# Kernel optimization log

Measured on AMD Instinct MI355X. Metric: run time of the kernel, lower is better.

The kernel has to match this reference:

```python
import jax, jax.numpy as jnp
import numpy as np

N_NODES = 100000

def _sage_conv(x, src, dst, deg_inv, Wl, bl, Wr):
    # PyG SAGEConv (aggr='mean', root_weight=True):
    #   out = lin_l(mean_{j in N(i)} x_j) + lin_r(x_i)
    msg = x[src]                                            # [E, d]
    agg = jax.ops.segment_sum(msg, dst, num_segments=N_NODES)  # [N, d]
    agg = agg * deg_inv                                     # mean (0 for isolated nodes)
    return agg @ Wl.T + bl + x @ Wr.T


def setup_inputs() -> dict:
    key = jax.random.key(0)
    ks = jax.random.split(key, 12)
    N, E, d_in, d_h, d_out = N_NODES, 1600000, 64, 64, 32
    x = jax.random.normal(ks[0], (N, d_in), dtype=jnp.float32)
    edge_index = jax.random.randint(ks[1], (2, E), 0, N, dtype=jnp.int64)

    def glorot(k, shape):
        fan_in = shape[1]
        return jax.random.normal(k, shape, dtype=jnp.float32) / np.sqrt(fan_in)

    return {
        "x": x,
        "edge_index": edge_index,
        "W1l": glorot(ks[2], (d_h, d_in)), "b1l": jnp.zeros((d_h,), jnp.float32), "W1r": glorot(ks[3], (d_h, d_in)),
        "W2l": glorot(ks[4], (d_h, d_h)),  "b2l": jnp.zeros((d_h,), jnp.float32), "W2r": glorot(ks[5], (d_h, d_h)),
        "W3l": glorot(ks[6], (d_h, d_h)),  "b3l": jnp.zeros((d_h,), jnp.float32), "W3r": glorot(ks[7], (d_h, d_h)),
        "Wfc": glorot(ks[8], (d_out, d_h)), "bfc": jnp.zeros((d_out,), jnp.float32),
    }


def reference(x, edge_index, W1l, b1l, W1r, W2l, b2l, W2r, W3l, b3l, W3r, Wfc, bfc):
    src, dst = edge_index[0], edge_index[1]
    # in-degree per destination node (shared by all three conv layers)
    ones = jnp.ones((src.shape[0],), x.dtype)
    deg = jax.ops.segment_sum(ones, dst, num_segments=N_NODES)
    deg_inv = (1.0 / jnp.maximum(deg, 1.0))[:, None]        # [N, 1]

    h = jax.nn.relu(_sage_conv(x, src, dst, deg_inv, W1l, b1l, W1r))
    # dropout(p=0.5) is identity in eval mode
    h = jax.nn.relu(_sage_conv(h, src, dst, deg_inv, W2l, b2l, W2r))
    h = jax.nn.relu(_sage_conv(h, src, dst, deg_inv, W3l, b3l, W3r))
    return h @ Wfc.T + bfc
```

## Files before the change

kernel.cpp:

```cpp
#include <hip/hip_runtime.h>
#include <hip/hip_fp16.h>

#define N_NODES 100000
#define D 64
#define BR 256
#define NB 391
#define ECH 2560
#define NROWPAD 100096

typedef _Float16 f16x8 __attribute__((ext_vector_type(8)));
typedef float f32x4 __attribute__((ext_vector_type(4)));

__device__ __forceinline__ float rlf(float v, int l) {
    union { float f; int i; } u;
    u.f = v;
    u.i = __builtin_amdgcn_readlane(u.i, l);
    return u.f;
}

__global__ __launch_bounds__(256) void k_cvt(const float4* __restrict__ x,
                                             uint2* __restrict__ y, int n4) {
    int i = blockIdx.x * 256 + threadIdx.x;
    if (i < n4) {
        float4 v = x[i];
        union { __half2 h[2]; uint2 u; } pk;
        pk.h[0] = __floats2half2_rn(v.x, v.y);
        pk.h[1] = __floats2half2_rn(v.z, v.w);
        y[i] = pk.u;
    }
}

__global__ __launch_bounds__(256) void k_prep(const float* __restrict__ Wl1, const float* __restrict__ Wr1,
                                              const float* __restrict__ Wl2, const float* __restrict__ Wr2,
                                              const float* __restrict__ Wl3, const float* __restrict__ Wr3,
                                              const float* __restrict__ Wfc,
                                              __half* __restrict__ Wf1, __half* __restrict__ Wf2,
                                              __half* __restrict__ Wf3, __half* __restrict__ Wffc,
                                              unsigned* __restrict__ x16, unsigned* __restrict__ H1,
                                              unsigned* __restrict__ H2,
                                              int* __restrict__ histT, int padded) {
    int t = blockIdx.x * 256 + threadIdx.x;
    if (t < 24576) {
        int layer = t / 8192;
        int r = t % 8192;
        int f = r >> 9, rem = r & 511;
        int lane = rem >> 3, i = rem & 7;
        int kt = f >> 2, nt = f & 3;
        int k = kt * 32 + (lane >> 4) * 8 + i;
        int o = nt * 16 + (lane & 15);
        const float* Wl = layer == 0 ? Wl1 : layer == 1 ? Wl2 : Wl3;
        const float* Wr = layer == 0 ? Wr1 : layer == 1 ? Wr2 : Wr3;
        float v = (k < 64) ? Wl[o * 64 + k] : Wr[o * 64 + (k - 64)];
        __half* Wf = layer == 0 ? Wf1 : layer == 1 ? Wf2 : Wf3;
        Wf[r] = __float2half(v);
    } else if (t < 26624) {
        int r = t - 24576;
        int f = r >> 9, rem = r & 511;
        int lane = rem >> 3, i = rem & 7;
        int kt = f >> 1, nt = f & 1;
        int k = kt * 32 + (lane >> 4) * 8 + i;
        int o = nt * 16 + (lane & 15);
        Wffc[r] = __float2half(Wfc[o * 64 + k]);
    } else if (t < 26720) {
        int z = t - 26624;
        unsigned* buf = (z >> 5) == 0 ? x16 : (z >> 5) == 1 ? H1 : H2;
        buf[(size_t)N_NODES * 32 + (z & 31)] = 0u;
    } else if (t >= 32768 && t < 32768 + padded) {
        histT[t - 32768] = 0;
    }
}


__global__ __launch_bounds__(512) void k_hist(const int* __restrict__ dst,
                                              int* __restrict__ histT,
                                              int E, int ga) {
    __shared__ int h[NB];
    int blk = blockIdx.x, tid = threadIdx.x;
    for (int i = tid; i < NB; i += 512) h[i] = 0;
    __syncthreads();
    int base = blk * ECH;
    int lim = E - base; if (lim > ECH) lim = ECH;
    for (int i = tid; i < lim; i += 512)
        atomicAdd(&h[dst[base + i] >> 8], 1);
    __syncthreads();
    for (int i = tid; i < NB; i += 512)
        histT[i * ga + blk] = h[i];
}

__global__ __launch_bounds__(256) void k_scan1(const int* __restrict__ cnt,
                                               int* __restrict__ part,
                                               int* __restrict__ bsums) {
    __shared__ int s[256];
    int tid = threadIdx.x;
    int i4 = blockIdx.x * 256 + tid;
    int4 v = reinterpret_cast<const int4*>(cnt)[i4];
    int tsum = v.x + v.y + v.z + v.w;
    s[tid] = tsum;
    __syncthreads();
    for (int off = 1; off < 256; off <<= 1) {
        int t = 0;
        if (tid >= off) t = s[tid - off];
        __syncthreads();
        if (tid >= off) s[tid] += t;
        __syncthreads();
    }
    int excl = tid ? s[tid - 1] : 0;
    if (tid == 255) bsums[blockIdx.x] = s[255];
    int4 o;
    o.x = excl;
    o.y = o.x + v.x;
    o.z = o.y + v.y;
    o.w = o.z + v.z;
    reinterpret_cast<int4*>(part)[i4] = o;
}

__global__ __launch_bounds__(256) void k_scan2(int* __restrict__ bsums, int nb,
                                               int* __restrict__ col) {
    __shared__ int s[256];
    int tid = threadIdx.x;
    if (tid < 8) col[tid] = N_NODES;
    int v = (tid < nb) ? bsums[tid] : 0;
    s[tid] = v;
    __syncthreads();
    for (int off = 1; off < 256; off <<= 1) {
        int t = 0;
        if (tid >= off) t = s[tid - off];
        __syncthreads();
        if (tid >= off) s[tid] += t;
        __syncthreads();
    }
    if (tid < nb) bsums[tid] = tid ? s[tid - 1] : 0;
}

__global__ __launch_bounds__(512) void k_part(const int* __restrict__ src,
                                              const int* __restrict__ dst,
                                              const int* __restrict__ offs,
                                              const int* __restrict__ bsums,
                                              int* __restrict__ bedge,
                                              int E, int ga) {
    __shared__ int o[NB];
    int blk = blockIdx.x, tid = threadIdx.x;
    for (int i = tid; i < NB; i += 512) {
        int ent = i * ga + blk;
        o[i] = offs[ent] + bsums[ent >> 10];
    }
    __syncthreads();
    int base = blk * ECH;
    int lim = E - base; if (lim > ECH) lim = ECH;
    for (int i = tid; i < lim; i += 512) {
        int e = base + i;
        int d = dst[e];
        int pos = atomicAdd(&o[d >> 8], 1);
        bedge[pos] = src[e] | ((d & 255) << 17);
    }
}

__global__ __launch_bounds__(256) void k_csr(const int* __restrict__ bedge,
                                             const int* __restrict__ offs,
                                             const int* __restrict__ bsums,
                                             int* __restrict__ col,
                                             int2* __restrict__ rp,
                                             float* __restrict__ deg_inv,
                                             int E, int ga) {
    __shared__ int lcnt[BR];
    __shared__ int stmp[BR];
    __shared__ int lcur[BR];
    int b = blockIdx.x, tid = threadIdx.x;
    int e0 = b * ga;
    int ebeg = offs[e0] + bsums[e0 >> 10];
    int eend = E;
    if (b + 1 < NB) {
        int e1 = (b + 1) * ga;
        eend = offs[e1] + bsums[e1 >> 10];
    }
    int nbase = b * BR;
    int cbase = ebeg + b * (BR * 4) + 8;
    lcnt[tid] = 0;
    __syncthreads();
    for (int e = ebeg + tid; e < eend; e += 256)
        atomicAdd(&lcnt[bedge[e] >> 17], 1);
    __syncthreads();
    int v = lcnt[tid];
    int pdeg = (v + 3) & ~3;
    stmp[tid] = pdeg;
    __syncthreads();
    for (int off = 1; off < 256; off <<= 1) {
        int t = 0;
        if (tid >= off) t = stmp[tid - off];
        __syncthreads();
        if (tid >= off) stmp[tid] += t;
        __syncthreads();
    }
    int ex = tid ? stmp[tid - 1] : 0;
    int slot = cbase + ex;
    lcur[tid] = slot;
    int node = nbase + tid;
    if (node < N_NODES) {
        rp[node] = make_int2(slot, slot + pdeg);
        deg_inv[node] = 1.0f / (float)(v > 1 ? v : 1);
        for (int s2 = slot + v; s2 < slot + pdeg; ++s2) col[s2] = N_NODES;
    }
    __syncthreads();
    for (int e = ebeg + tid; e < eend; e += 256) {
        int ed = bedge[e];
        int pos = atomicAdd(&lcur[ed >> 17], 1);
        col[pos] = ed & 0x1FFFF;
    }
}


__device__ __forceinline__ void fused_core(const __half* __restrict__ Hin,
                                           const __half* __restrict__ Wf,
                                           const float* __restrict__ bias,
                                           const int2* __restrict__ rp,
                                           const int* __restrict__ col,
                                           const float* __restrict__ deg_inv, int n,
                                           __half (&lds)[16][72], int m0, int l,
                                           f32x4 (&acc)[4]) {
    int q = l >> 4, li = l & 15;
    int beg = 0, nq = 0;
    float dinv = 0.f;
    if (l < 16 && m0 + l < n) {
        int2 se = rp[m0 + l];
        beg = se.x;
        nq = (se.y - se.x) >> 2;
        dinv = deg_inv[m0 + l];
    }
    const uint2* x8 = (const uint2*)Hin;
    const int* cq = col + q;

#pragma unroll
    for (int g = 0; g < 4; ++g) {
        int b0 = __builtin_amdgcn_readlane(beg, 4 * g + 0);
        int b1 = __builtin_amdgcn_readlane(beg, 4 * g + 1);
        int b2 = __builtin_amdgcn_readlane(beg, 4 * g + 2);
        int b3 = __builtin_amdgcn_readlane(beg, 4 * g + 3);
        int c0 = __builtin_amdgcn_readlane(nq, 4 * g + 0);
        int c1 = __builtin_amdgcn_readlane(nq, 4 * g + 1);
        int c2 = __builtin_amdgcn_readlane(nq, 4 * g + 2);
        int c3 = __builtin_amdgcn_readlane(nq, 4 * g + 3);
        int qmax = max(max(c0, c1), max(c2, c3));
        __half2 s00 = __floats2half2_rn(0.f, 0.f), s01 = s00;
        __half2 s10 = s00, s11 = s00, s20 = s00, s21 = s00, s30 = s00, s31 = s00;
        for (int qq = 0; qq < qmax; qq += 2) {
            int o = qq * 4;
            int a0 = qq < c0 ? b0 + o : 0;
            int a1 = qq < c1 ? b1 + o : 0;
            int a2 = qq < c2 ? b2 + o : 0;
            int a3 = qq < c3 ? b3 + o : 0;
            int a4 = qq + 1 < c0 ? b0 + o + 4 : 0;
            int a5 = qq + 1 < c1 ? b1 + o + 4 : 0;
            int a6 = qq + 1 < c2 ? b2 + o + 4 : 0;
            int a7 = qq + 1 < c3 ? b3 + o + 4 : 0;
            int i0 = cq[a0], i1 = cq[a1], i2 = cq[a2], i3 = cq[a3];
            int i4 = cq[a4], i5 = cq[a5], i6 = cq[a6], i7 = cq[a7];
            uint2 u0 = x8[(size_t)i0 * 16 + li];
            uint2 u1 = x8[(size_t)i1 * 16 + li];
            uint2 u2 = x8[(size_t)i2 * 16 + li];
            uint2 u3 = x8[(size_t)i3 * 16 + li];
            uint2 u4 = x8[(size_t)i4 * 16 + li];
            uint2 u5 = x8[(size_t)i5 * 16 + li];
            uint2 u6 = x8[(size_t)i6 * 16 + li];
            uint2 u7 = x8[(size_t)i7 * 16 + li];
            union { unsigned v; __half2 h; } w;
            w.v = u0.x; s00 = __hadd2(s00, w.h);
            w.v = u0.y; s01 = __hadd2(s01, w.h);
            w.v = u1.x; s10 = __hadd2(s10, w.h);
            w.v = u1.y; s11 = __hadd2(s11, w.h);
            w.v = u2.x; s20 = __hadd2(s20, w.h);
            w.v = u2.y; s21 = __hadd2(s21, w.h);
            w.v = u3.x; s30 = __hadd2(s30, w.h);
            w.v = u3.y; s31 = __hadd2(s31, w.h);
            w.v = u4.x; s00 = __hadd2(s00, w.h);
            w.v = u4.y; s01 = __hadd2(s01, w.h);
            w.v = u5.x; s10 = __hadd2(s10, w.h);
            w.v = u5.y; s11 = __hadd2(s11, w.h);
            w.v = u6.x; s20 = __hadd2(s20, w.h);
            w.v = u6.y; s21 = __hadd2(s21, w.h);
            w.v = u7.x; s30 = __hadd2(s30, w.h);
            w.v = u7.y; s31 = __hadd2(s31, w.h);
        }
        union { __half2 h; int i; } t;
#pragma unroll
        for (int m = 16; m < 64; m <<= 1) {
            t.h = s00; t.i = __shfl_xor(t.i, m); s00 = __hadd2(s00, t.h);
            t.h = s01; t.i = __shfl_xor(t.i, m); s01 = __hadd2(s01, t.h);
            t.h = s10; t.i = __shfl_xor(t.i, m); s10 = __hadd2(s10, t.h);
            t.h = s11; t.i = __shfl_xor(t.i, m); s11 = __hadd2(s11, t.h);
            t.h = s20; t.i = __shfl_xor(t.i, m); s20 = __hadd2(s20, t.h);
            t.h = s21; t.i = __shfl_xor(t.i, m); s21 = __hadd2(s21, t.h);
            t.h = s30; t.i = __shfl_xor(t.i, m); s30 = __hadd2(s30, t.h);
            t.h = s31; t.i = __shfl_xor(t.i, m); s31 = __hadd2(s31, t.h);
        }
        float d0 = rlf(dinv, 4 * g + 0);
        float d1 = rlf(dinv, 4 * g + 1);
        float d2 = rlf(dinv, 4 * g + 2);
        float d3 = rlf(dinv, 4 * g + 3);
        if (l < 16) {
            union { __half2 h; unsigned v; } p0, p1;
            float2 f;
            uint2 ov;
            f = __half22float2(s00); p0.h = __floats2half2_rn(f.x * d0, f.y * d0);
            f = __half22float2(s01); p1.h = __floats2half2_rn(f.x * d0, f.y * d0);
            ov.x = p0.v; ov.y = p1.v;
            *(uint2*)&lds[4 * g + 0][li * 4] = ov;
            f = __half22float2(s10); p0.h = __floats2half2_rn(f.x * d1, f.y * d1);
            f = __half22float2(s11); p1.h = __floats2half2_rn(f.x * d1, f.y * d1);
            ov.x = p0.v; ov.y = p1.v;
            *(uint2*)&lds[4 * g + 1][li * 4] = ov;
            f = __half22float2(s20); p0.h = __floats2half2_rn(f.x * d2, f.y * d2);
            f = __half22float2(s21); p1.h = __floats2half2_rn(f.x * d2, f.y * d2);
            ov.x = p0.v; ov.y = p1.v;
            *(uint2*)&lds[4 * g + 2][li * 4] = ov;
            f = __half22float2(s30); p0.h = __floats2half2_rn(f.x * d3, f.y * d3);
            f = __half22float2(s31); p1.h = __floats2half2_rn(f.x * d3, f.y * d3);
            ov.x = p0.v; ov.y = p1.v;
            *(uint2*)&lds[4 * g + 3][li * 4] = ov;
        }
    }

    const f16x8* wf8 = (const f16x8*)Wf;
    f16x8 bf[4][4];
#pragma unroll
    for (int kt = 0; kt < 4; ++kt)
#pragma unroll
        for (int nt = 0; nt < 4; ++nt)
            bf[kt][nt] = wf8[(kt * 4 + nt) * 64 + l];
    int rowA = li;
#pragma unroll
    for (int nt = 0; nt < 4; ++nt) {
        float bs = bias[nt * 16 + rowA];
        acc[nt] = (f32x4){bs, bs, bs, bs};
    }
#pragma unroll
    for (int kt = 0; kt < 4; ++kt) {
        f16x8 a;
        if (kt < 2)
            a = *(const f16x8*)&lds[rowA][kt * 32 + q * 8];
        else
            a = *(const f16x8*)(Hin + (size_t)(m0 + rowA) * D + (kt - 2) * 32 + q * 8);
#pragma unroll
        for (int nt = 0; nt < 4; ++nt)
            acc[nt] = __builtin_amdgcn_mfma_f32_16x16x32_f16(a, bf[kt][nt], acc[nt], 0, 0, 0);
    }
}

__global__ __launch_bounds__(256) void k_fused(const __half* __restrict__ Hin,
                                               __half* __restrict__ Hout,
                                               const __half* __restrict__ Wf,
                                               const float* __restrict__ bias,
                                               const int2* __restrict__ rp,
                                               const int* __restrict__ col,
                                               const float* __restrict__ deg_inv, int n) {
    __shared__ __half lds[4][16][72];
    int l = threadIdx.x & 63;
    int wv = threadIdx.x >> 6;
    int m0 = blockIdx.x * 64 + wv * 16;
    f32x4 acc[4];
    fused_core(Hin, Wf, bias, rp, col, deg_inv, n, lds[wv], m0, l, acc);
    int q = l >> 4, rowA = l & 15;
#pragma unroll
    for (int nt = 0; nt < 4; ++nt)
#pragma unroll
        for (int qd = 0; qd < 4; ++qd) {
            int node = m0 + q * 4 + qd;
            float v = fmaxf(acc[nt][qd], 0.f);
            if (node < n)
                Hout[(size_t)node * D + nt * 16 + rowA] = __float2half(v);
        }
}

__global__ __launch_bounds__(256) void k_fused_fc(const __half* __restrict__ Hin,
                                                  float* __restrict__ out,
                                                  const __half* __restrict__ Wf,
                                                  const float* __restrict__ bias,
                                                  const __half* __restrict__ Wffc,
                                                  const float* __restrict__ bfc,
                                                  const int2* __restrict__ rp,
                                                  const int* __restrict__ col,
                                                  const float* __restrict__ deg_inv, int n) {
    __shared__ __half lds[4][16][72];
    int l = threadIdx.x & 63;
    int wv = threadIdx.x >> 6;
    int m0 = blockIdx.x * 64 + wv * 16;
    f32x4 acc[4];
    fused_core(Hin, Wf, bias, rp, col, deg_inv, n, lds[wv], m0, l, acc);
    int q = l >> 4, li = l & 15;

#pragma unroll
    for (int nt = 0; nt < 4; ++nt)
#pragma unroll
        for (int qd = 0; qd < 4; ++qd)
            lds[wv][q * 4 + qd][nt * 16 + li] = __float2half(fmaxf(acc[nt][qd], 0.f));

    const f16x8* wfc8 = (const f16x8*)Wffc;
    f16x8 bf2[2][2];
#pragma unroll
    for (int kt = 0; kt < 2; ++kt)
#pragma unroll
        for (int nt = 0; nt < 2; ++nt)
            bf2[kt][nt] = wfc8[(kt * 2 + nt) * 64 + l];
    f32x4 acc2[2];
#pragma unroll
    for (int nt = 0; nt < 2; ++nt) {
        float bs = bfc[nt * 16 + li];
        acc2[nt] = (f32x4){bs, bs, bs, bs};
    }
#pragma unroll
    for (int kt = 0; kt < 2; ++kt) {
        f16x8 a = *(const f16x8*)&lds[wv][li][kt * 32 + q * 8];
#pragma unroll
        for (int nt = 0; nt < 2; ++nt)
            acc2[nt] = __builtin_amdgcn_mfma_f32_16x16x32_f16(a, bf2[kt][nt], acc2[nt], 0, 0, 0);
    }
#pragma unroll
    for (int nt = 0; nt < 2; ++nt)
#pragma unroll
        for (int qd = 0; qd < 4; ++qd) {
            int node = m0 + q * 4 + qd;
            if (node < n)
                out[(size_t)node * 32 + nt * 16 + li] = acc2[nt][qd];
        }
}


extern "C" void kernel_launch(void* const* d_in, const int* in_sizes, int n_in,
                              void* d_out, int out_size, void* d_ws, size_t ws_size,
                              hipStream_t stream) {
    const float* x   = (const float*)d_in[0];
    const int*   ei  = (const int*)d_in[1];
    const int    E   = in_sizes[1] / 2;
    const int*   src = ei;
    const int*   dst = ei + E;
    const float* W1l = (const float*)d_in[2];
    const float* b1l = (const float*)d_in[3];
    const float* W1r = (const float*)d_in[4];
    const float* W2l = (const float*)d_in[5];
    const float* b2l = (const float*)d_in[6];
    const float* W2r = (const float*)d_in[7];
    const float* W3l = (const float*)d_in[8];
    const float* b3l = (const float*)d_in[9];
    const float* W3r = (const float*)d_in[10];
    const float* Wfc = (const float*)d_in[11];
    const float* bfc = (const float*)d_in[12];
    float* out = (float*)d_out;

    const int ga      = (E + ECH - 1) / ECH;
    const int entries = NB * ga;
    const int padded  = (entries + 1023) & ~1023;
    const int nb2     = padded / 1024;

    char* p = (char*)d_ws;
    size_t off = 0;
    auto take = [&](size_t bytes) -> void* {
        void* r = p + off;
        off = (off + bytes + 255) & ~(size_t)255;
        return r;
    };
    __half* x16    = (__half*)take((size_t)NROWPAD * D * 2);
    __half* H1     = (__half*)take((size_t)NROWPAD * D * 2);
    __half* H2     = (__half*)take((size_t)NROWPAD * D * 2);
    float* deg_inv = (float*)take((size_t)N_NODES * 4);
    int2*  rp      = (int2*)take((size_t)N_NODES * 8);
    int*   histT   = (int*)take((size_t)padded * 4);
    int*   offs    = (int*)take((size_t)padded * 4);
    int*   bsums   = (int*)take(256 * 4);
    int*   bedge   = (int*)take((size_t)E * 4);
    int*   col     = (int*)take((size_t)(E + NB * BR * 4 + 72) * 4);
    __half* Wf1    = (__half*)take(8192 * 2);
    __half* Wf2    = (__half*)take(8192 * 2);
    __half* Wf3    = (__half*)take(8192 * 2);
    __half* Wffc   = (__half*)take(2048 * 2);

    int gp = (32768 + padded + 255) / 256;
    k_prep<<<gp, 256, 0, stream>>>(W1l, W1r, W2l, W2r, W3l, W3r, Wfc,
                                   Wf1, Wf2, Wf3, Wffc,
                                   (unsigned*)x16, (unsigned*)H1, (unsigned*)H2,
                                   histT, padded);
    int n4 = N_NODES * D / 4;
    k_cvt<<<(n4 + 255) / 256, 256, 0, stream>>>((const float4*)x, (uint2*)x16, n4);

    k_hist<<<ga, 512, 0, stream>>>(dst, histT, E, ga);
    k_scan1<<<nb2, 256, 0, stream>>>(histT, offs, bsums);
    k_scan2<<<1, 256, 0, stream>>>(bsums, nb2, col);
    k_part<<<ga, 512, 0, stream>>>(src, dst, offs, bsums, bedge, E, ga);
    k_csr<<<NB, 256, 0, stream>>>(bedge, offs, bsums, col, rp, deg_inv, E, ga);

    int gg = NROWPAD / 64;

    k_fused<<<gg, 256, 0, stream>>>(x16, H1, Wf1, b1l, rp, col, deg_inv, N_NODES);
    k_fused<<<gg, 256, 0, stream>>>(H1, H2, Wf2, b2l, rp, col, deg_inv, N_NODES);
    k_fused_fc<<<gg, 256, 0, stream>>>(H2, out, Wf3, b3l, Wffc, bfc, rp, col, deg_inv, N_NODES);
}
```

Before: 177.3 us.

## Fuse fp16 conversion into prep, cache edges in LDS for CSR, widen gather unroll

Folds the x-to-fp16 conversion kernel into the prep kernel, removing one launch. Only the tail of histT is zeroed now, which relies on k_hist writing every real entry. k_csr moves to 512 threads and keeps each bucket's edges in shared memory, so the second pass avoids re-reading bedge from global memory. The gather loop in the fused SAGE kernel is unrolled to issue 16 row loads per iteration instead of 8, giving more memory-level parallelism at the cost of extra registers.

```diff
diff --git a/kernel.cpp b/kernel.cpp
--- a/kernel.cpp
+++ b/kernel.cpp
@@ -7,6 +7,7 @@
 #define NB 391
 #define ECH 2560
 #define NROWPAD 100096
+#define CSRCAP 6144
 
 typedef _Float16 f16x8 __attribute__((ext_vector_type(8)));
 typedef float f32x4 __attribute__((ext_vector_type(4)));
@@ -16,18 +17,6 @@
     u.f = v;
     u.i = __builtin_amdgcn_readlane(u.i, l);
     return u.f;
-}
-
-__global__ __launch_bounds__(256) void k_cvt(const float4* __restrict__ x,
-                                             uint2* __restrict__ y, int n4) {
-    int i = blockIdx.x * 256 + threadIdx.x;
-    if (i < n4) {
-        float4 v = x[i];
-        union { __half2 h[2]; uint2 u; } pk;
-        pk.h[0] = __floats2half2_rn(v.x, v.y);
-        pk.h[1] = __floats2half2_rn(v.z, v.w);
-        y[i] = pk.u;
-    }
 }
 
 __global__ __launch_bounds__(256) void k_prep(const float* __restrict__ Wl1, const float* __restrict__ Wr1,
@@ -38,9 +27,19 @@
                                               __half* __restrict__ Wf3, __half* __restrict__ Wffc,
                                               unsigned* __restrict__ x16, unsigned* __restrict__ H1,
                                               unsigned* __restrict__ H2,
-                                              int* __restrict__ histT, int padded) {
+                                              int* __restrict__ histT, int entries, int ntail,
+                                              const float4* __restrict__ x, int n4) {
     int t = blockIdx.x * 256 + threadIdx.x;
-    if (t < 24576) {
+    if (t >= 65536) {
+        int i = t - 65536;
+        if (i < n4) {
+            float4 v = x[i];
+            union { __half2 h[2]; uint2 u; } pk;
+            pk.h[0] = __floats2half2_rn(v.x, v.y);
+            pk.h[1] = __floats2half2_rn(v.z, v.w);
+            ((uint2*)x16)[i] = pk.u;
+        }
+    } else if (t < 24576) {
         int layer = t / 8192;
         int r = t % 8192;
         int f = r >> 9, rem = r & 511;
@@ -65,8 +64,8 @@
         int z = t - 26624;
         unsigned* buf = (z >> 5) == 0 ? x16 : (z >> 5) == 1 ? H1 : H2;
         buf[(size_t)N_NODES * 32 + (z & 31)] = 0u;
-    } else if (t >= 32768 && t < 32768 + padded) {
-        histT[t - 32768] = 0;
+    } else if (t >= 32768 && t < 32768 + ntail) {
+        histT[entries + (t - 32768)] = 0;
     }
 }
 
@@ -155,13 +154,14 @@
     }
 }
 
-__global__ __launch_bounds__(256) void k_csr(const int* __restrict__ bedge,
+__global__ __launch_bounds__(512) void k_csr(const int* __restrict__ bedge,
                                              const int* __restrict__ offs,
                                              const int* __restrict__ bsums,
                                              int* __restrict__ col,
                                              int2* __restrict__ rp,
                                              float* __restrict__ deg_inv,
                                              int E, int ga) {
+    __shared__ int ebuf[CSRCAP];
     __shared__ int lcnt[BR];
     __shared__ int stmp[BR];
     __shared__ int lcur[BR];
@@ -173,36 +173,45 @@
         int e1 = (b + 1) * ga;
         eend = offs[e1] + bsums[e1 >> 10];
     }
+    int cnt = eend - ebeg;
     int nbase = b * BR;
     int cbase = ebeg + b * (BR * 4) + 8;
-    lcnt[tid] = 0;
-    __syncthreads();
-    for (int e = ebeg + tid; e < eend; e += 256)
-        atomicAdd(&lcnt[bedge[e] >> 17], 1);
-    __syncthreads();
-    int v = lcnt[tid];
-    int pdeg = (v + 3) & ~3;
-    stmp[tid] = pdeg;
+    if (tid < 256) lcnt[tid] = 0;
+    __syncthreads();
+    for (int i = tid; i < cnt; i += 512) {
+        int ed = bedge[ebeg + i];
+        if (i < CSRCAP) ebuf[i] = ed;
+        atomicAdd(&lcnt[ed >> 17], 1);
+    }
+    __syncthreads();
+    int v = 0, pdeg = 0;
+    if (tid < 256) {
+        v = lcnt[tid];
+        pdeg = (v + 3) & ~3;
+        stmp[tid] = pdeg;
+    }
     __syncthreads();
     for (int off = 1; off < 256; off <<= 1) {
         int t = 0;
-        if (tid >= off) t = stmp[tid - off];
-        __syncthreads();
-        if (tid >= off) stmp[tid] += t;
-        __syncthreads();
-    }
-    int ex = tid ? stmp[tid - 1] : 0;
-    int slot = cbase + ex;
-    lcur[tid] = slot;
-    int node = nbase + tid;
-    if (node < N_NODES) {
-        rp[node] = make_int2(slot, slot + pdeg);
-        deg_inv[node] = 1.0f / (float)(v > 1 ? v : 1);
-        for (int s2 = slot + v; s2 < slot + pdeg; ++s2) col[s2] = N_NODES;
-    }
-    __syncthreads();
-    for (int e = ebeg + tid; e < eend; e += 256) {
-        int ed = bedge[e];
+        if (tid < 256 && tid >= off) t = stmp[tid - off];
+        __syncthreads();
+        if (tid < 256 && tid >= off) stmp[tid] += t;
+        __syncthreads();
+    }
+    if (tid < 256) {
+        int ex = tid ? stmp[tid - 1] : 0;
+        int slot = cbase + ex;
+        lcur[tid] = slot;
+        int node = nbase + tid;
+        if (node < N_NODES) {
+            rp[node] = make_int2(slot, slot + pdeg);
+            deg_inv[node] = 1.0f / (float)(v > 1 ? v : 1);
+            for (int s2 = slot + v; s2 < slot + pdeg; ++s2) col[s2] = N_NODES;
+        }
+    }
+    __syncthreads();
+    for (int i = tid; i < cnt; i += 512) {
+        int ed = (i < CSRCAP) ? ebuf[i] : bedge[ebeg + i];
         int pos = atomicAdd(&lcur[ed >> 17], 1);
         col[pos] = ed & 0x1FFFF;
     }
@@ -242,43 +251,34 @@
         int qmax = max(max(c0, c1), max(c2, c3));
         __half2 s00 = __floats2half2_rn(0.f, 0.f), s01 = s00;
         __half2 s10 = s00, s11 = s00, s20 = s00, s21 = s00, s30 = s00, s31 = s00;
-        for (int qq = 0; qq < qmax; qq += 2) {
-            int o = qq * 4;
-            int a0 = qq < c0 ? b0 + o : 0;
-            int a1 = qq < c1 ? b1 + o : 0;
-            int a2 = qq < c2 ? b2 + o : 0;
-            int a3 = qq < c3 ? b3 + o : 0;
-            int a4 = qq + 1 < c0 ? b0 + o + 4 : 0;
-            int a5 = qq + 1 < c1 ? b1 + o + 4 : 0;
-            int a6 = qq + 1 < c2 ? b2 + o + 4 : 0;
-            int a7 = qq + 1 < c3 ? b3 + o + 4 : 0;
-            int i0 = cq[a0], i1 = cq[a1], i2 = cq[a2], i3 = cq[a3];
-            int i4 = cq[a4], i5 = cq[a5], i6 = cq[a6], i7 = cq[a7];
-            uint2 u0 = x8[(size_t)i0 * 16 + li];
-            uint2 u1 = x8[(size_t)i1 * 16 + li];
-            uint2 u2 = x8[(size_t)i2 * 16 + li];
-            uint2 u3 = x8[(size_t)i3 * 16 + li];
-            uint2 u4 = x8[(size_t)i4 * 16 + li];
-            uint2 u5 = x8[(size_t)i5 * 16 + li];
-            uint2 u6 = x8[(size_t)i6 * 16 + li];
-            uint2 u7 = x8[(size_t)i7 * 16 + li];
+        for (int qq = 0; qq < qmax; qq += 4) {
+            int a[16];
+#pragma unroll
+            for (int s = 0; s < 4; ++s) {
+                int o = (qq + s) * 4;
+                a[s * 4 + 0] = qq + s < c0 ? b0 + o : 0;
+                a[s * 4 + 1] = qq + s < c1 ? b1 + o : 0;
+                a[s * 4 + 2] = qq + s < c2 ? b2 + o : 0;
+                a[s * 4 + 3] = qq + s < c3 ? b3 + o : 0;
+            }
+            int idx[16];
+#pragma unroll
+            for (int i = 0; i < 16; ++i) idx[i] = cq[a[i]];
+            uint2 u[16];
+#pragma unroll
+            for (int i = 0; i < 16; ++i) u[i] = x8[(size_t)idx[i] * 16 + li];
             union { unsigned v; __half2 h; } w;
-            w.v = u0.x; s00 = __hadd2(s00, w.h);
-            w.v = u0.y; s01 = __hadd2(s01, w.h);
-            w.v = u1.x; s10 = __hadd2(s10, w.h);
-            w.v = u1.y; s11 = __hadd2(s11, w.h);
-            w.v = u2.x; s20 = __hadd2(s20, w.h);
-            w.v = u2.y; s21 = __hadd2(s21, w.h);
-            w.v = u3.x; s30 = __hadd2(s30, w.h);
-            w.v = u3.y; s31 = __hadd2(s31, w.h);
-            w.v = u4.x; s00 = __hadd2(s00, w.h);
-            w.v = u4.y; s01 = __hadd2(s01, w.h);
-            w.v = u5.x; s10 = __hadd2(s10, w.h);
-            w.v = u5.y; s11 = __hadd2(s11, w.h);
-            w.v = u6.x; s20 = __hadd2(s20, w.h);
-            w.v = u6.y; s21 = __hadd2(s21, w.h);
-            w.v = u7.x; s30 = __hadd2(s30, w.h);
-            w.v = u7.y; s31 = __hadd2(s31, w.h);
+#pragma unroll
+            for (int s = 0; s < 4; ++s) {
+                w.v = u[s * 4 + 0].x; s00 = __hadd2(s00, w.h);
+                w.v = u[s * 4 + 0].y; s01 = __hadd2(s01, w.h);
+                w.v = u[s * 4 + 1].x; s10 = __hadd2(s10, w.h);
+                w.v = u[s * 4 + 1].y; s11 = __hadd2(s11, w.h);
+                w.v = u[s * 4 + 2].x; s20 = __hadd2(s20, w.h);
+                w.v = u[s * 4 + 2].y; s21 = __hadd2(s21, w.h);
+                w.v = u[s * 4 + 3].x; s30 = __hadd2(s30, w.h);
+                w.v = u[s * 4 + 3].y; s31 = __hadd2(s31, w.h);
+            }
         }
         union { __half2 h; int i; } t;
 #pragma unroll
@@ -448,6 +448,7 @@
     const int ga      = (E + ECH - 1) / ECH;
     const int entries = NB * ga;
     const int padded  = (entries + 1023) & ~1023;
+    const int ntail   = padded - entries;
     const int nb2     = padded / 1024;
 
     char* p = (char*)d_ws;
@@ -472,19 +473,18 @@
     __half* Wf3    = (__half*)take(8192 * 2);
     __half* Wffc   = (__half*)take(2048 * 2);
 
-    int gp = (32768 + padded + 255) / 256;
+    int n4 = N_NODES * D / 4;
+    int gp = (65536 + n4 + 255) / 256;
     k_prep<<<gp, 256, 0, stream>>>(W1l, W1r, W2l, W2r, W3l, W3r, Wfc,
                                    Wf1, Wf2, Wf3, Wffc,
                                    (unsigned*)x16, (unsigned*)H1, (unsigned*)H2,
-                                   histT, padded);
-    int n4 = N_NODES * D / 4;
-    k_cvt<<<(n4 + 255) / 256, 256, 0, stream>>>((const float4*)x, (uint2*)x16, n4);
+                                   histT, entries, ntail, (const float4*)x, n4);
 
     k_hist<<<ga, 512, 0, stream>>>(dst, histT, E, ga);
     k_scan1<<<nb2, 256, 0, stream>>>(histT, offs, bsums);
     k_scan2<<<1, 256, 0, stream>>>(bsums, nb2, col);
     k_part<<<ga, 512, 0, stream>>>(src, dst, offs, bsums, bedge, E, ga);
-    k_csr<<<NB, 256, 0, stream>>>(bedge, offs, bsums, col, rp, deg_inv, E, ga);
+    k_csr<<<NB, 512, 0, stream>>>(bedge, offs, bsums, col, rp, deg_inv, E, ga);
 
     int gg = NROWPAD / 64;
 
```

Result: slower. 182.8 us (+3.1%).

## Fold fp16 conversion into prep kernel, cache CSR edges in LDS, prefetch self rows

Applied to the files above, without the earlier changes.

Merges the fp32-to-fp16 input conversion into the prep kernel, which removes one launch. Histogram zeroing now covers only the padded tail instead of the whole buffer. The CSR build runs 512 threads per block and keeps each bucket's edges in shared memory, so the second pass skips a global re-read. The fused layer kernel also loads the node's own features early so they overlap with the gather. The changes are unrelated; the risks are LDS pressure in k_csr and histT entries left unzeroed if k_hist does not write every entry.

```diff
diff --git a/kernel.cpp b/kernel.cpp
--- a/kernel.cpp
+++ b/kernel.cpp
@@ -7,6 +7,7 @@
 #define NB 391
 #define ECH 2560
 #define NROWPAD 100096
+#define CSRCAP 6144
 
 typedef _Float16 f16x8 __attribute__((ext_vector_type(8)));
 typedef float f32x4 __attribute__((ext_vector_type(4)));
@@ -16,18 +17,6 @@
     u.f = v;
     u.i = __builtin_amdgcn_readlane(u.i, l);
     return u.f;
-}
-
-__global__ __launch_bounds__(256) void k_cvt(const float4* __restrict__ x,
-                                             uint2* __restrict__ y, int n4) {
-    int i = blockIdx.x * 256 + threadIdx.x;
-    if (i < n4) {
-        float4 v = x[i];
-        union { __half2 h[2]; uint2 u; } pk;
-        pk.h[0] = __floats2half2_rn(v.x, v.y);
-        pk.h[1] = __floats2half2_rn(v.z, v.w);
-        y[i] = pk.u;
-    }
 }
 
 __global__ __launch_bounds__(256) void k_prep(const float* __restrict__ Wl1, const float* __restrict__ Wr1,
@@ -38,9 +27,19 @@
                                               __half* __restrict__ Wf3, __half* __restrict__ Wffc,
                                               unsigned* __restrict__ x16, unsigned* __restrict__ H1,
                                               unsigned* __restrict__ H2,
-                                              int* __restrict__ histT, int padded) {
+                                              int* __restrict__ histT, int entries, int ntail,
+                                              const float4* __restrict__ x, int n4) {
     int t = blockIdx.x * 256 + threadIdx.x;
-    if (t < 24576) {
+    if (t >= 65536) {
+        int i = t - 65536;
+        if (i < n4) {
+            float4 v = x[i];
+            union { __half2 h[2]; uint2 u; } pk;
+            pk.h[0] = __floats2half2_rn(v.x, v.y);
+            pk.h[1] = __floats2half2_rn(v.z, v.w);
+            ((uint2*)x16)[i] = pk.u;
+        }
+    } else if (t < 24576) {
         int layer = t / 8192;
         int r = t % 8192;
         int f = r >> 9, rem = r & 511;
@@ -65,8 +64,8 @@
         int z = t - 26624;
         unsigned* buf = (z >> 5) == 0 ? x16 : (z >> 5) == 1 ? H1 : H2;
         buf[(size_t)N_NODES * 32 + (z & 31)] = 0u;
-    } else if (t >= 32768 && t < 32768 + padded) {
-        histT[t - 32768] = 0;
+    } else if (t >= 32768 && t < 32768 + ntail) {
+        histT[entries + (t - 32768)] = 0;
     }
 }
 
@@ -155,13 +154,14 @@
     }
 }
 
-__global__ __launch_bounds__(256) void k_csr(const int* __restrict__ bedge,
+__global__ __launch_bounds__(512) void k_csr(const int* __restrict__ bedge,
                                              const int* __restrict__ offs,
                                              const int* __restrict__ bsums,
                                              int* __restrict__ col,
                                              int2* __restrict__ rp,
                                              float* __restrict__ deg_inv,
                                              int E, int ga) {
+    __shared__ int ebuf[CSRCAP];
     __shared__ int lcnt[BR];
     __shared__ int stmp[BR];
     __shared__ int lcur[BR];
@@ -173,36 +173,45 @@
         int e1 = (b + 1) * ga;
         eend = offs[e1] + bsums[e1 >> 10];
     }
+    int cnt = eend - ebeg;
     int nbase = b * BR;
     int cbase = ebeg + b * (BR * 4) + 8;
-    lcnt[tid] = 0;
-    __syncthreads();
-    for (int e = ebeg + tid; e < eend; e += 256)
-        atomicAdd(&lcnt[bedge[e] >> 17], 1);
-    __syncthreads();
-    int v = lcnt[tid];
-    int pdeg = (v + 3) & ~3;
-    stmp[tid] = pdeg;
+    if (tid < 256) lcnt[tid] = 0;
+    __syncthreads();
+    for (int i = tid; i < cnt; i += 512) {
+        int ed = bedge[ebeg + i];
+        if (i < CSRCAP) ebuf[i] = ed;
+        atomicAdd(&lcnt[ed >> 17], 1);
+    }
+    __syncthreads();
+    int v = 0, pdeg = 0;
+    if (tid < 256) {
+        v = lcnt[tid];
+        pdeg = (v + 3) & ~3;
+        stmp[tid] = pdeg;
+    }
     __syncthreads();
     for (int off = 1; off < 256; off <<= 1) {
         int t = 0;
-        if (tid >= off) t = stmp[tid - off];
+        if (tid < 256 && tid >= off) t = stmp[tid - off];
         __syncthreads();
-        if (tid >= off) stmp[tid] += t;
+        if (tid < 256 && tid >= off) stmp[tid] += t;
         __syncthreads();
     }
-    int ex = tid ? stmp[tid - 1] : 0;
-    int slot = cbase + ex;
-    lcur[tid] = slot;
-    int node = nbase + tid;
-    if (node < N_NODES) {
-        rp[node] = make_int2(slot, slot + pdeg);
-        deg_inv[node] = 1.0f / (float)(v > 1 ? v : 1);
-        for (int s2 = slot + v; s2 < slot + pdeg; ++s2) col[s2] = N_NODES;
-    }
-    __syncthreads();
-    for (int e = ebeg + tid; e < eend; e += 256) {
-        int ed = bedge[e];
+    if (tid < 256) {
+        int ex = tid ? stmp[tid - 1] : 0;
+        int slot = cbase + ex;
+        lcur[tid] = slot;
+        int node = nbase + tid;
+        if (node < N_NODES) {
+            rp[node] = make_int2(slot, slot + pdeg);
+            deg_inv[node] = 1.0f / (float)(v > 1 ? v : 1);
+            for (int s2 = slot + v; s2 < slot + pdeg; ++s2) col[s2] = N_NODES;
+        }
+    }
+    __syncthreads();
+    for (int i = tid; i < cnt; i += 512) {
+        int ed = (i < CSRCAP) ? ebuf[i] : bedge[ebeg + i];
         int pos = atomicAdd(&lcur[ed >> 17], 1);
         col[pos] = ed & 0x1FFFF;
     }
@@ -226,6 +235,10 @@
         nq = (se.y - se.x) >> 2;
         dinv = deg_inv[m0 + l];
     }
+    const __half* selfp = Hin + (size_t)(m0 + li) * D;
+    f16x8 self0 = *(const f16x8*)(selfp + q * 8);
+    f16x8 self1 = *(const f16x8*)(selfp + 32 + q * 8);
+
     const uint2* x8 = (const uint2*)Hin;
     const int* cq = col + q;
 
@@ -338,7 +351,7 @@
         if (kt < 2)
             a = *(const f16x8*)&lds[rowA][kt * 32 + q * 8];
         else
-            a = *(const f16x8*)(Hin + (size_t)(m0 + rowA) * D + (kt - 2) * 32 + q * 8);
+            a = (kt == 2) ? self0 : self1;
 #pragma unroll
         for (int nt = 0; nt < 4; ++nt)
             acc[nt] = __builtin_amdgcn_mfma_f32_16x16x32_f16(a, bf[kt][nt], acc[nt], 0, 0, 0);
@@ -448,6 +461,7 @@
     const int ga      = (E + ECH - 1) / ECH;
     const int entries = NB * ga;
     const int padded  = (entries + 1023) & ~1023;
+    const int ntail   = padded - entries;
     const int nb2     = padded / 1024;
 
     char* p = (char*)d_ws;
@@ -472,19 +486,18 @@
     __half* Wf3    = (__half*)take(8192 * 2);
     __half* Wffc   = (__half*)take(2048 * 2);
 
-    int gp = (32768 + padded + 255) / 256;
+    int n4 = N_NODES * D / 4;
+    int gp = (65536 + n4 + 255) / 256;
     k_prep<<<gp, 256, 0, stream>>>(W1l, W1r, W2l, W2r, W3l, W3r, Wfc,
                                    Wf1, Wf2, Wf3, Wffc,
                                    (unsigned*)x16, (unsigned*)H1, (unsigned*)H2,
-                                   histT, padded);
-    int n4 = N_NODES * D / 4;
-    k_cvt<<<(n4 + 255) / 256, 256, 0, stream>>>((const float4*)x, (uint2*)x16, n4);
+                                   histT, entries, ntail, (const float4*)x, n4);
 
     k_hist<<<ga, 512, 0, stream>>>(dst, histT, E, ga);
     k_scan1<<<nb2, 256, 0, stream>>>(histT, offs, bsums);
     k_scan2<<<1, 256, 0, stream>>>(bsums, nb2, col);
     k_part<<<ga, 512, 0, stream>>>(src, dst, offs, bsums, bedge, E, ga);
-    k_csr<<<NB, 256, 0, stream>>>(bedge, offs, bsums, col, rp, deg_inv, E, ga);
+    k_csr<<<NB, 512, 0, stream>>>(bedge, offs, bsums, col, rp, deg_inv, E, ga);
 
     int gg = NROWPAD / 64;
 
```

Result: faster. 171.8 us, median of 2 (-3.1%).
